# Kernel tuning notes

Hardware: AMD Instinct MI355X
Metric: run time of the kernel (lower is better)

Reference implementation:

```python
import jax, jax.numpy as jnp
import numpy as np

GAMMA = 0.9


def setup_inputs() -> dict:
    key = jax.random.key(0)
    k1, k2 = jax.random.split(key)
    B, H, W, C, D = 1, 32, 32, 8, 64
    num_heads = 8
    head_dim = D // num_heads  # 8, must equal C for the module's broadcasting
    x = jax.random.normal(k1, (B, H, W, C, D), dtype=jnp.float32)
    decay = jnp.ones((1, num_heads, 1, 1, 1), dtype=jnp.float32)  # base_decay=1.0
    spec_pe = jax.random.normal(k2, (1, num_heads, 1, 1, head_dim), dtype=jnp.float32)
    return {"x": x, "decay": decay, "spec_pe": spec_pe}


def _manhattan_mask(H, W, C, dtype):
    # dist[h1,w1,c1,h2,w2,c2] = |h1-h2| + |w1-w2| + |c1-c2|
    # Built from per-axis |delta| tables to avoid the (H,W,C,H,W,C,3) intermediate.
    dh = jnp.abs(jnp.arange(H)[:, None] - jnp.arange(H)[None, :])  # (H,H)
    dw = jnp.abs(jnp.arange(W)[:, None] - jnp.arange(W)[None, :])  # (W,W)
    dc = jnp.abs(jnp.arange(C)[:, None] - jnp.arange(C)[None, :])  # (C,C)
    dist = (dh[:, None, None, :, None, None]
            + dw[None, :, None, None, :, None]
            + dc[None, None, :, None, None, :])  # (H,W,C,H,W,C)
    mask = jnp.asarray(GAMMA, dtype) ** dist.astype(dtype)
    return mask[None, None]  # (1,1,H,W,C,H,W,C)


def reference(x, decay, spec_pe):
    B, H, W, C, D = x.shape
    mask = _manhattan_mask(H, W, C, x.dtype)            # (1,1,H,W,C,H,W,C)
    mean = jnp.mean(mask, axis=(5, 6, 7), keepdims=True)  # (1,1,H,W,C,1,1,1)
    # spec_pe (1,nh,1,1,Dh) broadcasts against trailing dims (requires nh==C, Dh==C)
    spec = spec_pe * mean
    mask = mask * (1.0 + spec)
    mask = mask * decay  # decay (1,nh,1,1,1) broadcasts at dim -4 (nh==C)
    return mask
```

## Files before the change

kernel.cpp:

```cpp
#include <hip/hip_runtime.h>


constexpr int TOTAL_F4 = 16777216;

__global__ __launch_bounds__(256) void manhattan_relpos_kernel(
    const float* __restrict__ decay,
    const float* __restrict__ spec_pe,
    float* __restrict__ out)
{
    __shared__ float powtab[72];
    __shared__ float Sh[32];
    __shared__ float meanC[8];
    __shared__ float A[64];
    __shared__ float SP[64];

    const int tid = threadIdx.x;

    if (tid < 72) {
        powtab[tid] = exp2f((float)tid * -0.15200309344504997f);
    }
    __syncthreads();
    if (tid < 32) {
        float s = 0.0f;
        #pragma unroll
        for (int j = 0; j < 32; ++j) s += powtab[abs(tid - j)];
        Sh[tid] = s;
    } else if (tid < 40) {
        const int c1 = tid - 32;
        float s = 0.0f;
        #pragma unroll
        for (int j = 0; j < 8; ++j) s += powtab[abs(c1 - j)];
        meanC[c1] = s * (1.0f / 8192.0f);
    } else if (tid >= 64 && tid < 128) {
        const int i = tid - 64;
        const int c1 = i >> 3, c2 = i & 7;
        A[i]  = powtab[abs(c1 - c2)] * decay[c1];
        SP[i] = spec_pe[i];
    }
    __syncthreads();

    const int stride = gridDim.x * blockDim.x;
    for (int idx = blockIdx.x * blockDim.x + tid; idx < TOTAL_F4; idx += stride) {
        const int half = idx & 1;
        const int w2 = (idx >> 1)  & 31;
        const int h2 = (idx >> 6)  & 31;
        const int c1 = (idx >> 11) & 7;
        const int w1 = (idx >> 14) & 31;
        const int h1 = (idx >> 19) & 31;

        const float p = powtab[abs(h1 - h2) + abs(w1 - w2)];
        const float m = Sh[h1] * Sh[w1] * meanC[c1];
        const int cbase = (c1 << 3) + (half << 2);

        float4 v;
        v.x = p * A[cbase + 0] * fmaf(SP[cbase + 0], m, 1.0f);
        v.y = p * A[cbase + 1] * fmaf(SP[cbase + 1], m, 1.0f);
        v.z = p * A[cbase + 2] * fmaf(SP[cbase + 2], m, 1.0f);
        v.w = p * A[cbase + 3] * fmaf(SP[cbase + 3], m, 1.0f);
        reinterpret_cast<float4*>(out)[idx] = v;
    }
}

extern "C" void kernel_launch(void* const* d_in, const int* in_sizes, int n_in,
                              void* d_out, int out_size, void* d_ws, size_t ws_size,
                              hipStream_t stream) {
    const float* decay   = (const float*)d_in[1];
    const float* spec_pe = (const float*)d_in[2];
    float* out = (float*)d_out;

    dim3 grid(8192), block(256);
    manhattan_relpos_kernel<<<grid, block, 0, stream>>>(decay, spec_pe, out);
}
```

Before: 256.8 us.

## Map one block per output slice and factor the h-decay out of the inner loop

Each block now handles a fixed (h1,w1,c1) slice of 2048 float4 outputs instead of looping grid-stride. Per-thread constants (the w-decay times coefficient times spec factor) are computed once, and each of 8 unrolled stores multiplies only by the h-distance power. This cuts per-element index math and shared-memory lookups in a store-bound kernel. The kernel relies on grid size 8192 and block size 256 matching the output shape exactly.

```diff
diff --git a/kernel.cpp b/kernel.cpp
--- a/kernel.cpp
+++ b/kernel.cpp
@@ -1,7 +1,5 @@
 #include <hip/hip_runtime.h>
 
-
-constexpr int TOTAL_F4 = 16777216;
 
 __global__ __launch_bounds__(256) void manhattan_relpos_kernel(
     const float* __restrict__ decay,
@@ -39,25 +37,35 @@
     }
     __syncthreads();
 
-    const int stride = gridDim.x * blockDim.x;
-    for (int idx = blockIdx.x * blockDim.x + tid; idx < TOTAL_F4; idx += stride) {
-        const int half = idx & 1;
-        const int w2 = (idx >> 1)  & 31;
-        const int h2 = (idx >> 6)  & 31;
-        const int c1 = (idx >> 11) & 7;
-        const int w1 = (idx >> 14) & 31;
-        const int h1 = (idx >> 19) & 31;
+    const int slice = blockIdx.x;
+    const int c1 = slice & 7;
+    const int w1 = (slice >> 3) & 31;
+    const int h1 = slice >> 8;
 
-        const float p = powtab[abs(h1 - h2) + abs(w1 - w2)];
-        const float m = Sh[h1] * Sh[w1] * meanC[c1];
-        const int cbase = (c1 << 3) + (half << 2);
+    const int half = tid & 1;
+    const int w2   = (tid >> 1) & 31;
+    const int h2lo = tid >> 6;
 
+    const float pw = powtab[abs(w1 - w2)];
+    const float m  = Sh[h1] * Sh[w1] * meanC[c1];
+    const int cbase = (c1 << 3) + (half << 2);
+
+    const float K0 = pw * A[cbase + 0] * fmaf(SP[cbase + 0], m, 1.0f);
+    const float K1 = pw * A[cbase + 1] * fmaf(SP[cbase + 1], m, 1.0f);
+    const float K2 = pw * A[cbase + 2] * fmaf(SP[cbase + 2], m, 1.0f);
+    const float K3 = pw * A[cbase + 3] * fmaf(SP[cbase + 3], m, 1.0f);
+
+    float4* outp = reinterpret_cast<float4*>(out) + slice * 2048 + tid;
+    #pragma unroll
+    for (int i = 0; i < 8; ++i) {
+        const int h2 = (i << 2) | h2lo;
+        const float ph = powtab[abs(h1 - h2)];
         float4 v;
-        v.x = p * A[cbase + 0] * fmaf(SP[cbase + 0], m, 1.0f);
-        v.y = p * A[cbase + 1] * fmaf(SP[cbase + 1], m, 1.0f);
-        v.z = p * A[cbase + 2] * fmaf(SP[cbase + 2], m, 1.0f);
-        v.w = p * A[cbase + 3] * fmaf(SP[cbase + 3], m, 1.0f);
-        reinterpret_cast<float4*>(out)[idx] = v;
+        v.x = ph * K0;
+        v.y = ph * K1;
+        v.z = ph * K2;
+        v.w = ph * K3;
+        outp[i << 8] = v;
     }
 }
 
```

Result: no change. 258.5 us (+0.7%).

## Factor mask into separable per-axis terms and drop shared-memory tables

Applied to the files above, without the earlier changes.

Replaces the grid-stride loop with a fixed mapping where each block owns one (h1,w1,half of c1) slice and each thread writes 32 float4s along h2. The per-axis sums use a closed-form geometric series instead of a shared-memory reduction, and the output is written as a per-thread product of h-decay and a precomputed w/c factor. This removes both __syncthreads, the shared-memory lookups and the index decoding. It costs more registers per thread and hard-codes the output shape. The kernel is a pure 256 MB write, so it is likely already store-bound.

```diff
diff --git a/kernel.cpp b/kernel.cpp
--- a/kernel.cpp
+++ b/kernel.cpp
@@ -1,63 +1,56 @@
 #include <hip/hip_runtime.h>
 
 
-constexpr int TOTAL_F4 = 16777216;
+constexpr float L2G = -0.15200309344504997f;
 
-__global__ __launch_bounds__(256) void manhattan_relpos_kernel(
+__global__ __launch_bounds__(256, 8) void manhattan_relpos_fill(
     const float* __restrict__ decay,
     const float* __restrict__ spec_pe,
     float* __restrict__ out)
 {
-    __shared__ float powtab[72];
-    __shared__ float Sh[32];
-    __shared__ float meanC[8];
-    __shared__ float A[64];
-    __shared__ float SP[64];
+    const int tid  = threadIdx.x;
+    const int lane = tid & 63;
+    const int wave = tid >> 6;
+    const int blk  = blockIdx.x;
 
-    const int tid = threadIdx.x;
+    const int half = lane & 1;
+    const int w2   = lane >> 1;
+    const int c1   = wave | ((blk & 1) << 2);
+    const int w1   = (blk >> 1) & 31;
+    const int h1   = blk >> 6;
 
-    if (tid < 72) {
-        powtab[tid] = exp2f((float)tid * -0.15200309344504997f);
+    const float Sh1 = 19.0f - 9.0f * (exp2f((float)h1 * L2G) + exp2f((float)(31 - h1) * L2G));
+    const float Sw1 = 19.0f - 9.0f * (exp2f((float)w1 * L2G) + exp2f((float)(31 - w1) * L2G));
+    const float Sc1 = 19.0f - 9.0f * (exp2f((float)c1 * L2G) + exp2f((float)(7  - c1) * L2G));
+    const float m   = Sh1 * Sw1 * Sc1 * (1.0f / 8192.0f);
+
+    const float pw  = exp2f(fabsf((float)(w1 - w2)) * L2G);
+    const float dec = decay[c1];
+
+    float K[4];
+    #pragma unroll
+    for (int j = 0; j < 4; ++j) {
+        const int c2   = (half << 2) + j;
+        const float pc = exp2f(fabsf((float)(c1 - c2)) * L2G);
+        const float sp = spec_pe[(c1 << 3) + c2];
+        K[j] = pw * pc * dec * fmaf(sp, m, 1.0f);
     }
-    __syncthreads();
-    if (tid < 32) {
-        float s = 0.0f;
-        #pragma unroll
-        for (int j = 0; j < 32; ++j) s += powtab[abs(tid - j)];
-        Sh[tid] = s;
-    } else if (tid < 40) {
-        const int c1 = tid - 32;
-        float s = 0.0f;
-        #pragma unroll
-        for (int j = 0; j < 8; ++j) s += powtab[abs(c1 - j)];
-        meanC[c1] = s * (1.0f / 8192.0f);
-    } else if (tid >= 64 && tid < 128) {
-        const int i = tid - 64;
-        const int c1 = i >> 3, c2 = i & 7;
-        A[i]  = powtab[abs(c1 - c2)] * decay[c1];
-        SP[i] = spec_pe[i];
-    }
-    __syncthreads();
 
-    const int stride = gridDim.x * blockDim.x;
-    for (int idx = blockIdx.x * blockDim.x + tid; idx < TOTAL_F4; idx += stride) {
-        const int half = idx & 1;
-        const int w2 = (idx >> 1)  & 31;
-        const int h2 = (idx >> 6)  & 31;
-        const int c1 = (idx >> 11) & 7;
-        const int w1 = (idx >> 14) & 31;
-        const int h1 = (idx >> 19) & 31;
+    float ph[32];
+    #pragma unroll
+    for (int i = 0; i < 32; ++i)
+        ph[i] = exp2f(fabsf((float)(h1 - i)) * L2G);
 
-        const float p = powtab[abs(h1 - h2) + abs(w1 - w2)];
-        const float m = Sh[h1] * Sh[w1] * meanC[c1];
-        const int cbase = (c1 << 3) + (half << 2);
-
+    float4* outp = reinterpret_cast<float4*>(out)
+                 + ((size_t)blk << 13) + (wave << 11) + lane;
+    #pragma unroll
+    for (int i = 0; i < 32; ++i) {
         float4 v;
-        v.x = p * A[cbase + 0] * fmaf(SP[cbase + 0], m, 1.0f);
-        v.y = p * A[cbase + 1] * fmaf(SP[cbase + 1], m, 1.0f);
-        v.z = p * A[cbase + 2] * fmaf(SP[cbase + 2], m, 1.0f);
-        v.w = p * A[cbase + 3] * fmaf(SP[cbase + 3], m, 1.0f);
-        reinterpret_cast<float4*>(out)[idx] = v;
+        v.x = ph[i] * K[0];
+        v.y = ph[i] * K[1];
+        v.z = ph[i] * K[2];
+        v.w = ph[i] * K[3];
+        outp[i << 6] = v;
     }
 }
 
@@ -68,6 +61,6 @@
     const float* spec_pe = (const float*)d_in[2];
     float* out = (float*)d_out;
 
-    dim3 grid(8192), block(256);
-    manhattan_relpos_kernel<<<grid, block, 0, stream>>>(decay, spec_pe, out);
+    dim3 grid(2048), block(256);
+    manhattan_relpos_fill<<<grid, block, 0, stream>>>(decay, spec_pe, out);
 }
```

New measurement: 279.6 us. 1.09x slower.
